# Optimization experiments

Hardware: AMD Instinct MI355X
Metric: run time of the kernel (lower is better)

Reference implementation:

```python
import jax, jax.numpy as jnp
import numpy as np

IN_FEATURES = 1024
OUT_FEATURES = 1024
KNOT_COUNT = 5
ORDER = 3
BATCH = 4096


def setup_inputs() -> dict:
    key = jax.random.key(0)
    k1, k2 = jax.random.split(key)
    x = jax.random.normal(k1, (BATCH, IN_FEATURES), dtype=jnp.float32)
    knots = jnp.linspace(-1.0, 1.0, KNOT_COUNT, dtype=jnp.float32)
    coeffs = jax.random.normal(k2, (KNOT_COUNT + ORDER, OUT_FEATURES, IN_FEATURES), dtype=jnp.float32)
    return {"x": x, "knots": knots, "coeffs": coeffs}


def _bspline_bases(x, knots, order):
    # x: [B, I]; knots: [K] uniform grid. Extend to K + 2*order + 1 knots so
    # the number of degree-`order` basis functions is K + order.
    h = knots[1] - knots[0]
    left = knots[0] + h * jnp.arange(-order, 0, dtype=knots.dtype)
    right = knots[-1] + h * jnp.arange(1, order + 2, dtype=knots.dtype)
    t = jnp.concatenate([left, knots, right])  # [K + 2*order + 1]
    xe = x[..., None]  # [B, I, 1]
    # degree-0 indicator bases: [B, I, m-1]
    bases = ((xe >= t[:-1]) & (xe < t[1:])).astype(x.dtype)
    # Cox-de Boor recursion up to degree `order` (vectorized over batch/features)
    for k in range(1, order + 1):
        left_num = (xe - t[: -(k + 1)]) / (t[k:-1] - t[: -(k + 1)])
        right_num = (t[k + 1:] - xe) / (t[k + 1:] - t[1:-k])
        bases = left_num * bases[..., :-1] + right_num * bases[..., 1:]
    return bases  # [B, I, K + order]


def reference(x, knots, coeffs):
    # Faithful fused version of the per-(i,j) python loops:
    # spline_j(b) = sum_n B_n(x[b,i]) * coeffs[n, j, i]; output sums over i.
    bases = _bspline_bases(x, knots, ORDER)          # [B, I, N]
    return jnp.einsum('bin,noi->bo', bases, coeffs)  # [B, O]
```

## Files before the change

kernel.cpp:

```cpp
#include <hip/hip_runtime.h>
#include <hip/hip_bf16.h>
#include <cstdint>
#include <cstddef>

#define IN_F   1024
#define OUT_F  1024
#define NB     8
#define BATCH  4096
#define KTOT   (NB * IN_F)

typedef __attribute__((ext_vector_type(4)))  float  f32x4;
typedef __attribute__((ext_vector_type(8)))  float  f32x8;
typedef __attribute__((ext_vector_type(8)))  __bf16 bf16x8;

#define GLDS16(g, l)                                                     \
    __builtin_amdgcn_global_load_lds(                                    \
        (const __attribute__((address_space(1))) void*)(g),              \
        (__attribute__((address_space(3))) void*)(l), 16, 0, 0)

__device__ __forceinline__ void spline_w(float r, float w[4]) {
    const float r2 = r * r, r3 = r2 * r;
    const float omr = 1.0f - r;
    w[0] = omr * omr * omr * (1.0f / 6.0f);
    w[1] = (3.0f * r3 - 6.0f * r2 + 4.0f) * (1.0f / 6.0f);
    w[2] = (-3.0f * r3 + 3.0f * r2 + 3.0f * r + 1.0f) * (1.0f / 6.0f);
    w[3] = r3 * (1.0f / 6.0f);
}

__global__ void k_prep(const float* __restrict__ coeffs, __bf16* __restrict__ Wb,
                       const float* __restrict__ x, __bf16* __restrict__ A) {
    const int bb = blockIdx.x;
    if (bb < 4096) {
        const size_t g   = (size_t)bb * blockDim.x + threadIdx.x;
        const size_t idx = g * 8;
        const int i = (int)(idx & 1023);
        const int o = (int)((idx >> 10) & 1023);
        const int c = (i >> 3) & 7;
        const int isw = (i & ~63) | ((c ^ (o & 7)) << 3);
        f32x8 v = *(const f32x8*)(coeffs + idx);
        bf16x8 ov = __builtin_convertvector(v, bf16x8);
        *(bf16x8*)(Wb + (idx - i) + isw) = ov;
    } else {
        const int g    = (bb - 4096) * blockDim.x + threadIdx.x;
        const int flat = g * 8;
        const int b = flat >> 10, i = flat & 1023;
        f32x8 xv = *(const f32x8*)(x + flat);

        float w[8][4];
        int   jj[8];
#pragma unroll
        for (int e = 0; e < 8; ++e) {
            const float u  = (xv[e] + 2.5f) * 2.0f;
            const float jf = floorf(u);
            jj[e] = (int)jf;
            spline_w(u - jf, w[e]);
        }

        const int c   = (i >> 3) & 7;
        const int isw = (i & ~63) | ((c ^ (b & 7)) << 3);
        __bf16* base = A + (size_t)b * KTOT + isw;
#pragma unroll
        for (int n = 0; n < NB; ++n) {
            bf16x8 pack;
#pragma unroll
            for (int e = 0; e < 8; ++e) {
                const int d = n - jj[e] + 3;
                float v = (d == 0) ? w[e][0]
                        : (d == 1) ? w[e][1]
                        : (d == 2) ? w[e][2]
                        : (d == 3) ? w[e][3] : 0.0f;
                pack[e] = (__bf16)v;
            }
            *(bf16x8*)(base + n * IN_F) = pack;
        }
    }
}

#define BM 256
#define BN 128
#define BK 64
#define NT (KTOT / BK)
#define SPLITK 2
#define NTS (NT / SPLITK)
#define BUFSZ 49152

__global__ __launch_bounds__(512) void k_gemm(const __bf16* __restrict__ A,
                                              const __bf16* __restrict__ W,
                                              float* __restrict__ C,
                                              float* __restrict__ P) {
    __shared__ __align__(16) char ls[3 * BUFSZ];

    const int fid = blockIdx.x;
    const int xcd = fid & 7;
    const int s   = fid >> 3;
    const int y   = xcd + 8 * (s & 1);
    const int xb  = (s >> 1) & 7;
    const int kz  = s >> 4;

    const int o0   = xb * BN;
    const int b0   = y * BM;
    const int tid  = threadIdx.x;
    const int lane = tid & 63;
    const int wv   = tid >> 6;
    const int wr   = wv >> 1;
    const int wc   = wv & 1;
    const int l15  = lane & 15;
    const int lhi  = lane >> 4;

    f32x4 acc[4][4] = {};

    const int srow  = tid >> 3;
    const int scol8 = (tid & 7) * 8;

    auto STAGE = [&](int buf, int kt) {
        const int k0 = kt * BK;
        const int n  = k0 >> 10;
        const int i0 = k0 & 1023;
        char* la = ls + buf * BUFSZ;
        char* lb = la + 32768;
#pragma unroll
        for (int it = 0; it < 4; ++it) {
            const __bf16* ga = A + (size_t)(b0 + srow + it * 64) * KTOT + k0 + scol8;
            GLDS16(ga, la + tid * 16 + it * 8192);
        }
#pragma unroll
        for (int it = 0; it < 2; ++it) {
            const __bf16* gw = W + ((size_t)n << 20)
                                 + (size_t)(o0 + srow + it * 64) * IN_F + i0 + scol8;
            GLDS16(gw, lb + tid * 16 + it * 8192);
        }
    };

    const int ktBeg = kz * NTS;
    STAGE(0, ktBeg);
    STAGE(1, ktBeg + 1);

    int cur = 0, nxt = 2;
    for (int t = 0; t < NTS; ++t) {
        if (t < NTS - 1) asm volatile("s_waitcnt vmcnt(6)" ::: "memory");
        else             asm volatile("s_waitcnt vmcnt(0)" ::: "memory");
        __builtin_amdgcn_s_barrier();
        __builtin_amdgcn_sched_barrier(0);

        if (t + 2 < NTS) STAGE(nxt, ktBeg + t + 2);

        const char* la = ls + cur * BUFSZ;
        const char* lb = la + 32768;
#pragma unroll
        for (int kk = 0; kk < BK; kk += 32) {
            bf16x8 af[4], bfr[4];
#pragma unroll
            for (int m = 0; m < 4; ++m) {
                const int r = wr * 64 + m * 16 + l15;
                const int c = ((kk >> 3) + lhi) ^ (r & 7);
                af[m] = *(const bf16x8*)(la + r * 128 + c * 16);
            }
#pragma unroll
            for (int nn = 0; nn < 4; ++nn) {
                const int r = wc * 64 + nn * 16 + l15;
                const int c = ((kk >> 3) + lhi) ^ (r & 7);
                bfr[nn] = *(const bf16x8*)(lb + r * 128 + c * 16);
            }
            __builtin_amdgcn_s_setprio(1);
#pragma unroll
            for (int m = 0; m < 4; ++m)
#pragma unroll
                for (int nn = 0; nn < 4; ++nn)
                    acc[m][nn] = __builtin_amdgcn_mfma_f32_16x16x32_bf16(
                        af[m], bfr[nn], acc[m][nn], 0, 0, 0);
            __builtin_amdgcn_s_setprio(0);
        }
        cur = (cur == 2) ? 0 : cur + 1;
        nxt = (nxt == 2) ? 0 : nxt + 1;
    }

    float* dst = (kz == 0) ? C : P;
    const int crow = lhi * 4;
#pragma unroll
    for (int m = 0; m < 4; ++m) {
#pragma unroll
        for (int nn = 0; nn < 4; ++nn) {
            float* cp = dst + (size_t)(b0 + wr * 64 + m * 16 + crow) * OUT_F
                            + o0 + wc * 64 + nn * 16 + l15;
#pragma unroll
            for (int j = 0; j < 4; ++j)
                cp[(size_t)j * OUT_F] = acc[m][nn][j];
        }
    }
}

__global__ void k_add(float* __restrict__ C, const float* __restrict__ P) {
    const size_t g = (size_t)(blockIdx.x * blockDim.x + threadIdx.x) * 4;
    f32x4 a = *(const f32x4*)(C + g);
    f32x4 b = *(const f32x4*)(P + g);
    a += b;
    *(f32x4*)(C + g) = a;
}

__global__ void k_naive(const float* __restrict__ x, const float* __restrict__ coeffs,
                        float* __restrict__ out) {
    const int b = blockIdx.y * 16 + (threadIdx.x >> 4);
    const int o = blockIdx.x * 16 + (threadIdx.x & 15);
    float sum = 0.0f;
    for (int i = 0; i < IN_F; ++i) {
        const float u  = (x[(size_t)b * IN_F + i] + 2.5f) * 2.0f;
        const float jf = floorf(u);
        const int   j  = (int)jf;
        float w[4];
        spline_w(u - jf, w);
#pragma unroll
        for (int m = 0; m < 4; ++m) {
            const int idx = j - 3 + m;
            if (idx >= 0 && idx < NB)
                sum += w[m] * coeffs[(size_t)idx * OUT_F * IN_F + (size_t)o * IN_F + i];
        }
    }
    out[(size_t)b * OUT_F + o] = sum;
}

extern "C" void kernel_launch(void* const* d_in, const int* in_sizes, int n_in,
                              void* d_out, int out_size, void* d_ws, size_t ws_size,
                              hipStream_t stream) {
    const float* x      = (const float*)d_in[0];
    const float* coeffs = (const float*)d_in[2];
    float* out = (float*)d_out;

    const size_t needA = (size_t)BATCH * KTOT * sizeof(__bf16);
    const size_t needW = (size_t)NB * OUT_F * IN_F * sizeof(__bf16);
    const size_t oneP  = (size_t)BATCH * OUT_F * sizeof(float);

    if (ws_size >= needA + needW + oneP) {
        __bf16* A  = (__bf16*)d_ws;
        __bf16* Wb = (__bf16*)((char*)d_ws + needA);
        float*  P  = (float*)((char*)d_ws + needA + needW);

        hipLaunchKernelGGL(k_prep, dim3(6144), dim3(256), 0, stream,
                           coeffs, Wb, x, A);
        hipLaunchKernelGGL(k_gemm, dim3(256), dim3(512), 0, stream,
                           A, Wb, out, P);
        hipLaunchKernelGGL(k_add, dim3(BATCH * OUT_F / 4 / 256), dim3(256),
                           0, stream, out, P);
    } else {
        hipLaunchKernelGGL(k_naive, dim3(OUT_F / 16, BATCH / 16), dim3(256), 0,
                           stream, x, coeffs, out);
    }
}
```

Before: 121.5 us.

## Quantize spline bases and coefficients to int8 and use int8 MFMA

Replaces the bf16 GEMM path with int8. Coefficients are quantized per (basis, output) row with a stored scale, and spline basis values use a fixed scale. The GEMM uses the i8 16x16x64 MFMA and accumulates int32 per basis slice, then rescales into fp32 accumulators. This halves workspace traffic and LDS footprint and doubles MFMA throughput per instruction, but the int8 rounding of weights and basis values adds error that may exceed the tolerance. It also drops the LDS XOR swizzle, which may cause bank conflicts.

```diff
diff --git a/kernel.cpp b/kernel.cpp
--- a/kernel.cpp
+++ b/kernel.cpp
@@ -11,12 +11,16 @@
 
 typedef __attribute__((ext_vector_type(4)))  float  f32x4;
 typedef __attribute__((ext_vector_type(8)))  float  f32x8;
-typedef __attribute__((ext_vector_type(8)))  __bf16 bf16x8;
+typedef __attribute__((ext_vector_type(4)))  int    i32x4;
 
 #define GLDS16(g, l)                                                     \
     __builtin_amdgcn_global_load_lds(                                    \
         (const __attribute__((address_space(1))) void*)(g),              \
         (__attribute__((address_space(3))) void*)(l), 16, 0, 0)
+
+#define FENCE() __builtin_amdgcn_sched_barrier(0)
+
+#define SA 190.5f
 
 __device__ __forceinline__ void spline_w(float r, float w[4]) {
     const float r2 = r * r, r3 = r2 * r;
@@ -27,21 +31,42 @@
     w[3] = r3 * (1.0f / 6.0f);
 }
 
-__global__ void k_prep(const float* __restrict__ coeffs, __bf16* __restrict__ Wb,
-                       const float* __restrict__ x, __bf16* __restrict__ A) {
-    const int bb = blockIdx.x;
-    if (bb < 4096) {
-        const size_t g   = (size_t)bb * blockDim.x + threadIdx.x;
-        const size_t idx = g * 8;
-        const int i = (int)(idx & 1023);
-        const int o = (int)((idx >> 10) & 1023);
-        const int c = (i >> 3) & 7;
-        const int isw = (i & ~63) | ((c ^ (o & 7)) << 3);
-        f32x8 v = *(const f32x8*)(coeffs + idx);
-        bf16x8 ov = __builtin_convertvector(v, bf16x8);
-        *(bf16x8*)(Wb + (idx - i) + isw) = ov;
+__global__ void k_prep(const float* __restrict__ coeffs, signed char* __restrict__ W8,
+                       float* __restrict__ sW,
+                       const float* __restrict__ x, signed char* __restrict__ A8) {
+    const int bb  = blockIdx.x;
+    const int tid = threadIdx.x;
+    if (bb < 2048) {
+        const int r    = bb * 4 + (tid >> 6);
+        const int lane = tid & 63;
+        const float* src = coeffs + (size_t)r * 1024 + lane * 16;
+        f32x4 v[4];
+#pragma unroll
+        for (int e = 0; e < 4; ++e) v[e] = ((const f32x4*)src)[e];
+        float am = 0.0f;
+#pragma unroll
+        for (int e = 0; e < 4; ++e)
+#pragma unroll
+            for (int j = 0; j < 4; ++j) am = fmaxf(am, fabsf(v[e][j]));
+#pragma unroll
+        for (int m = 1; m < 64; m <<= 1) am = fmaxf(am, __shfl_xor(am, m));
+        am = fmaxf(am, 1e-20f);
+        const float inv = 127.0f / am;
+        i32x4 o;
+#pragma unroll
+        for (int e = 0; e < 4; ++e) {
+            unsigned int u = 0;
+#pragma unroll
+            for (int j = 0; j < 4; ++j) {
+                const int q = (int)__builtin_rintf(v[e][j] * inv);
+                u |= ((unsigned int)(q & 255)) << (8 * j);
+            }
+            o[e] = (int)u;
+        }
+        *(i32x4*)(W8 + (size_t)r * 1024 + lane * 16) = o;
+        if (lane == 0) sW[r] = am / (127.0f * SA);
     } else {
-        const int g    = (bb - 4096) * blockDim.x + threadIdx.x;
+        const int g    = (bb - 2048) * blockDim.x + tid;
         const int flat = g * 8;
         const int b = flat >> 10, i = flat & 1023;
         f32x8 xv = *(const f32x8*)(x + flat);
@@ -56,12 +81,10 @@
             spline_w(u - jf, w[e]);
         }
 
-        const int c   = (i >> 3) & 7;
-        const int isw = (i & ~63) | ((c ^ (b & 7)) << 3);
-        __bf16* base = A + (size_t)b * KTOT + isw;
+        signed char* base = A8 + (size_t)b * KTOT + i;
 #pragma unroll
         for (int n = 0; n < NB; ++n) {
-            bf16x8 pack;
+            unsigned long long u64 = 0;
 #pragma unroll
             for (int e = 0; e < 8; ++e) {
                 const int d = n - jj[e] + 3;
@@ -69,9 +92,10 @@
                         : (d == 1) ? w[e][1]
                         : (d == 2) ? w[e][2]
                         : (d == 3) ? w[e][3] : 0.0f;
-                pack[e] = (__bf16)v;
+                const int q = (int)__builtin_rintf(v * SA);
+                u64 |= ((unsigned long long)(q & 255)) << (8 * e);
             }
-            *(bf16x8*)(base + n * IN_F) = pack;
+            *(unsigned long long*)(base + n * IN_F) = u64;
         }
     }
 }
@@ -82,12 +106,13 @@
 #define NT (KTOT / BK)
 #define SPLITK 2
 #define NTS (NT / SPLITK)
-#define BUFSZ 49152
-
-__global__ __launch_bounds__(512) void k_gemm(const __bf16* __restrict__ A,
-                                              const __bf16* __restrict__ W,
-                                              float* __restrict__ C,
-                                              float* __restrict__ P) {
+#define BUFSZ 24576
+
+__global__ __launch_bounds__(512, 4) void k_gemm(const signed char* __restrict__ A8,
+                                                 const signed char* __restrict__ W8,
+                                                 const float* __restrict__ sW,
+                                                 float* __restrict__ C,
+                                                 float* __restrict__ P) {
     __shared__ __align__(16) char ls[3 * BUFSZ];
 
     const int fid = blockIdx.x;
@@ -107,71 +132,79 @@
     const int l15  = lane & 15;
     const int lhi  = lane >> 4;
 
-    f32x4 acc[4][4] = {};
-
-    const int srow  = tid >> 3;
-    const int scol8 = (tid & 7) * 8;
+    f32x4 accf[4][4] = {};
+    i32x4 acci[4][4] = {};
+
+    const int srow = tid >> 2;
+    const int scol = (tid & 3) * 16;
 
     auto STAGE = [&](int buf, int kt) {
         const int k0 = kt * BK;
         const int n  = k0 >> 10;
         const int i0 = k0 & 1023;
         char* la = ls + buf * BUFSZ;
-        char* lb = la + 32768;
-#pragma unroll
-        for (int it = 0; it < 4; ++it) {
-            const __bf16* ga = A + (size_t)(b0 + srow + it * 64) * KTOT + k0 + scol8;
-            GLDS16(ga, la + tid * 16 + it * 8192);
-        }
-#pragma unroll
-        for (int it = 0; it < 2; ++it) {
-            const __bf16* gw = W + ((size_t)n << 20)
-                                 + (size_t)(o0 + srow + it * 64) * IN_F + i0 + scol8;
-            GLDS16(gw, lb + tid * 16 + it * 8192);
-        }
+        char* lb = la + 16384;
+        GLDS16(A8 + (size_t)(b0 + srow) * KTOT + k0 + scol,       la + tid * 16);
+        GLDS16(A8 + (size_t)(b0 + srow + 128) * KTOT + k0 + scol, la + tid * 16 + 8192);
+        GLDS16(W8 + ((size_t)n << 20) + (size_t)(o0 + srow) * IN_F + i0 + scol,
+               lb + tid * 16);
     };
+
+    float sWr[4][4];
+#pragma unroll
+    for (int sl = 0; sl < 4; ++sl)
+#pragma unroll
+        for (int nn = 0; nn < 4; ++nn)
+            sWr[sl][nn] = sW[(size_t)(kz * 4 + sl) * 1024
+                             + o0 + wc * 64 + nn * 16 + l15];
+    FENCE();
+    asm volatile("s_waitcnt vmcnt(0)" ::: "memory");
+    FENCE();
 
     const int ktBeg = kz * NTS;
     STAGE(0, ktBeg);
     STAGE(1, ktBeg + 1);
 
     int cur = 0, nxt = 2;
-    for (int t = 0; t < NTS; ++t) {
-        if (t < NTS - 1) asm volatile("s_waitcnt vmcnt(6)" ::: "memory");
-        else             asm volatile("s_waitcnt vmcnt(0)" ::: "memory");
-        __builtin_amdgcn_s_barrier();
-        __builtin_amdgcn_sched_barrier(0);
-
-        if (t + 2 < NTS) STAGE(nxt, ktBeg + t + 2);
-
-        const char* la = ls + cur * BUFSZ;
-        const char* lb = la + 32768;
-#pragma unroll
-        for (int kk = 0; kk < BK; kk += 32) {
-            bf16x8 af[4], bfr[4];
-#pragma unroll
-            for (int m = 0; m < 4; ++m) {
-                const int r = wr * 64 + m * 16 + l15;
-                const int c = ((kk >> 3) + lhi) ^ (r & 7);
-                af[m] = *(const bf16x8*)(la + r * 128 + c * 16);
+#pragma unroll
+    for (int sl = 0; sl < 4; ++sl) {
+        for (int tt = 0; tt < 16; ++tt) {
+            const int t = sl * 16 + tt;
+            if (t < NTS - 1) asm volatile("s_waitcnt vmcnt(3)" ::: "memory");
+            else             asm volatile("s_waitcnt vmcnt(0)" ::: "memory");
+            __builtin_amdgcn_s_barrier();
+            FENCE();
+
+            if (t + 2 < NTS) STAGE(nxt, ktBeg + t + 2);
+
+            const char* la = ls + cur * BUFSZ;
+            const char* lb = la + 16384;
+            i32x4 af[4], bfr[4];
+#pragma unroll
+            for (int m = 0; m < 4; ++m)
+                af[m] = *(const i32x4*)(la + (wr * 64 + m * 16 + l15) * 64 + lhi * 16);
+#pragma unroll
+            for (int nn = 0; nn < 4; ++nn)
+                bfr[nn] = *(const i32x4*)(lb + (wc * 64 + nn * 16 + l15) * 64 + lhi * 16);
+            __builtin_amdgcn_s_setprio(1);
+#pragma unroll
+            for (int m = 0; m < 4; ++m)
+#pragma unroll
+                for (int nn = 0; nn < 4; ++nn)
+                    acci[m][nn] = __builtin_amdgcn_mfma_i32_16x16x64_i8(
+                        af[m], bfr[nn], acci[m][nn], 0, 0, 0);
+            __builtin_amdgcn_s_setprio(0);
+            cur = (cur == 2) ? 0 : cur + 1;
+            nxt = (nxt == 2) ? 0 : nxt + 1;
+        }
+#pragma unroll
+        for (int m = 0; m < 4; ++m)
+#pragma unroll
+            for (int nn = 0; nn < 4; ++nn) {
+                accf[m][nn] += __builtin_convertvector(acci[m][nn], f32x4)
+                               * sWr[sl][nn];
+                acci[m][nn] = (i32x4){0, 0, 0, 0};
             }
-#pragma unroll
-            for (int nn = 0; nn < 4; ++nn) {
-                const int r = wc * 64 + nn * 16 + l15;
-                const int c = ((kk >> 3) + lhi) ^ (r & 7);
-                bfr[nn] = *(const bf16x8*)(lb + r * 128 + c * 16);
-            }
-            __builtin_amdgcn_s_setprio(1);
-#pragma unroll
-            for (int m = 0; m < 4; ++m)
-#pragma unroll
-                for (int nn = 0; nn < 4; ++nn)
-                    acc[m][nn] = __builtin_amdgcn_mfma_f32_16x16x32_bf16(
-                        af[m], bfr[nn], acc[m][nn], 0, 0, 0);
-            __builtin_amdgcn_s_setprio(0);
-        }
-        cur = (cur == 2) ? 0 : cur + 1;
-        nxt = (nxt == 2) ? 0 : nxt + 1;
     }
 
     float* dst = (kz == 0) ? C : P;
@@ -184,7 +217,7 @@
                             + o0 + wc * 64 + nn * 16 + l15;
 #pragma unroll
             for (int j = 0; j < 4; ++j)
-                cp[(size_t)j * OUT_F] = acc[m][nn][j];
+                cp[(size_t)j * OUT_F] = accf[m][nn][j];
         }
     }
 }
@@ -225,19 +258,21 @@
     const float* coeffs = (const float*)d_in[2];
     float* out = (float*)d_out;
 
-    const size_t needA = (size_t)BATCH * KTOT * sizeof(__bf16);
-    const size_t needW = (size_t)NB * OUT_F * IN_F * sizeof(__bf16);
+    const size_t needA = (size_t)BATCH * KTOT;
+    const size_t needW = (size_t)NB * OUT_F * IN_F;
+    const size_t needS = (size_t)NB * OUT_F * sizeof(float);
     const size_t oneP  = (size_t)BATCH * OUT_F * sizeof(float);
 
-    if (ws_size >= needA + needW + oneP) {
-        __bf16* A  = (__bf16*)d_ws;
-        __bf16* Wb = (__bf16*)((char*)d_ws + needA);
-        float*  P  = (float*)((char*)d_ws + needA + needW);
-
-        hipLaunchKernelGGL(k_prep, dim3(6144), dim3(256), 0, stream,
-                           coeffs, Wb, x, A);
+    if (ws_size >= needA + needW + needS + oneP) {
+        signed char* A8 = (signed char*)d_ws;
+        signed char* W8 = (signed char*)((char*)d_ws + needA);
+        float*       sW = (float*)((char*)d_ws + needA + needW);
+        float*       P  = (float*)((char*)d_ws + needA + needW + needS);
+
+        hipLaunchKernelGGL(k_prep, dim3(4096), dim3(256), 0, stream,
+                           coeffs, W8, sW, x, A8);
         hipLaunchKernelGGL(k_gemm, dim3(256), dim3(512), 0, stream,
-                           A, Wb, out, P);
+                           A8, W8, sW, out, P);
         hipLaunchKernelGGL(k_add, dim3(BATCH * OUT_F / 4 / 256), dim3(256),
                            0, stream, out, P);
     } else {
```

Result: slower. 151.9 us (+25.1%).
